# Performance work log

Measured on AMD Instinct MI355X. Metric: run time of the kernel, lower is better.

## Reference

```python
import jax, jax.numpy as jnp
import numpy as np

EPS_LN = 1e-5


def fwht(x):
    """Fast Walsh-Hadamard transform over the last axis (power-of-two length).
    Vectorized butterfly: log2(n) stages, each a reshape + add/sub."""
    orig_shape = x.shape
    n = orig_shape[-1]
    y = x.reshape(-1, n)
    h = 1
    while h < n:
        y = y.reshape(-1, n // (2 * h), 2, h)
        a = y[:, :, 0, :]
        b = y[:, :, 1, :]
        y = jnp.stack([a + b, a - b], axis=2).reshape(-1, n)
        h <<= 1
    return y.reshape(orig_shape)


def setup_inputs() -> dict:
    key = jax.random.key(0)
    kx, kw, kg = jax.random.split(key, 3)
    B, S, D_IN, D_OUT = 4, 4096, 2048, 2048
    x = jax.random.normal(kx, (B, S, D_IN), dtype=jnp.float32)
    # kaiming_uniform_(a=sqrt(5)) -> bound = 1/sqrt(in_features)
    bound = 1.0 / np.sqrt(D_IN)
    W = jax.random.uniform(kw, (D_OUT, D_IN), dtype=jnp.float32,
                           minval=-bound, maxval=bound)
    gamma = jnp.ones((D_IN,), dtype=jnp.float32)
    beta = jnp.zeros((D_IN,), dtype=jnp.float32)
    return {"x": x, "W": W, "gamma": gamma, "beta": beta}


def reference(x, W, gamma, beta):
    bits = 4
    max_val = (1 << (bits - 1)) - 1  # 7
    # LayerNorm over last dim
    mu = jnp.mean(x, axis=-1, keepdims=True)
    var = jnp.mean(jnp.square(x - mu), axis=-1, keepdims=True)
    x_ln = (x - mu) * jax.lax.rsqrt(var + EPS_LN) * gamma + beta
    # Activation fake-quant to `bits` bits (per-row absmax scale)
    x_scale = jnp.clip(jnp.max(jnp.abs(x_ln), axis=-1, keepdims=True), 1e-6, None)
    x_int = jnp.clip(jnp.round(x_ln * max_val / x_scale), -max_val, max_val)
    x_q = x_int * x_scale / max_val
    # Hadamard transform of quantized activations
    x_h = fwht(x_q)
    # Ternary weight quantization with global mean-abs scale
    w_scale = jnp.clip(jnp.mean(jnp.abs(W)), 1e-6, None)
    w_q = (jnp.where(W > 0.5 * w_scale, 1.0, 0.0)
           + jnp.where(W < -0.5 * w_scale, -1.0, 0.0)) * w_scale
    # Linear (no bias), then second Hadamard transform
    out = jnp.einsum('bsd,od->bso', x_h, w_q)
    return fwht(out)
```

## Files before the change

### kernel.cpp

```cpp
#include <hip/hip_runtime.h>

typedef unsigned short u16;
typedef __attribute__((ext_vector_type(8))) __bf16 bf16x8;
typedef __attribute__((ext_vector_type(4))) float floatx4;

#define DDIM 2048
#define MROWS 16384

__device__ __forceinline__ u16 f2bf(float f) {
    unsigned int u = __builtin_bit_cast(unsigned int, f);
    u = (u + 0x7fffu + ((u >> 16) & 1u)) >> 16;
    return (u16)u;
}

__device__ __forceinline__ float wave_sum(float v) {
#pragma unroll
    for (int o = 32; o > 0; o >>= 1) v += __shfl_down(v, o, 64);
    return v;
}
__device__ __forceinline__ float wave_max(float v) {
#pragma unroll
    for (int o = 32; o > 0; o >>= 1) v = fmaxf(v, __shfl_down(v, o, 64));
    return v;
}

__global__ __launch_bounds__(256) void absmean_part(const float4* __restrict__ W4,
                                                    float* __restrict__ partial) {
    float s = 0.f;
    for (int i = blockIdx.x * 256 + threadIdx.x; i < (DDIM * DDIM / 4); i += 1024 * 256) {
        float4 v = W4[i];
        s += fabsf(v.x) + fabsf(v.y) + fabsf(v.z) + fabsf(v.w);
    }
    s = wave_sum(s);
    __shared__ float red[4];
    if ((threadIdx.x & 63) == 0) red[threadIdx.x >> 6] = s;
    __syncthreads();
    if (threadIdx.x == 0) partial[blockIdx.x] = red[0] + red[1] + red[2] + red[3];
}

template <bool QUANT>
__global__ __launch_bounds__(256) void transpose_k(const float* __restrict__ in,
                                                   float* __restrict__ out,
                                                   const float* __restrict__ partial) {
    __shared__ float tile[64][65];
    const int t = threadIdx.x;
    float wsc = 0.f, half_t = 0.f;
    if (QUANT) {
        __shared__ float wred[4];
        float s = partial[t] + partial[t + 256] + partial[t + 512] + partial[t + 768];
        s = wave_sum(s);
        if ((t & 63) == 0) wred[t >> 6] = s;
        __syncthreads();
        float m = (wred[0] + wred[1] + wred[2] + wred[3]) * (1.0f / (float)(DDIM * DDIM));
        wsc = fmaxf(m, 1e-6f);
        half_t = 0.5f * wsc;
        __syncthreads();
    }
    const int tx = t & 63;
    const int ty = t >> 6;
    const int r0 = blockIdx.y * 64;
    const int c0 = blockIdx.x * 64;
#pragma unroll
    for (int i = 0; i < 16; ++i) {
        int r = ty + i * 4;
        float w = in[(size_t)(r0 + r) * DDIM + c0 + tx];
        if (QUANT) w = (w > half_t ? wsc : 0.f) + (w < -half_t ? -wsc : 0.f);
        tile[r][tx] = w;
    }
    __syncthreads();
#pragma unroll
    for (int i = 0; i < 16; ++i) {
        int r = ty + i * 4;
        out[(size_t)(c0 + r) * DDIM + r0 + tx] = tile[tx][r];
    }
}

template <bool BF16OUT>
__global__ __launch_bounds__(256) void fwht_rows(const float* __restrict__ in,
                                                 void* __restrict__ out) {
    __shared__ float s0[DDIM];
    __shared__ float s1[DDIM];
    const int row = blockIdx.x;
    const int t = threadIdx.x;
    const int lane = t & 63;
    const float4* rp = (const float4*)(in + (size_t)row * DDIM);
    float4 a = rp[t], b = rp[t + 256];
    float v[8] = {a.x, a.y, a.z, a.w, b.x, b.y, b.z, b.w};

#pragma unroll
    for (int h = 1; h <= 4; h <<= 1)
#pragma unroll
        for (int j = 0; j < 8; ++j)
            if (!(j & h)) { float x = v[j], y = v[j | h]; v[j] = x + y; v[j | h] = x - y; }

#pragma unroll
    for (int m = 1; m <= 32; m <<= 1)
#pragma unroll
        for (int j = 0; j < 8; ++j) {
            float p = __shfl_xor(v[j], m, 64);
            v[j] = (lane & m) ? (p - v[j]) : (p + v[j]);
        }

    ((float4*)s0)[2 * t] = make_float4(v[0], v[1], v[2], v[3]);
    ((float4*)s0)[2 * t + 1] = make_float4(v[4], v[5], v[6], v[7]);
    __syncthreads();
    {
        int p1 = t ^ 64;
        float4 pa = ((const float4*)s0)[2 * p1], pb = ((const float4*)s0)[2 * p1 + 1];
        float pv[8] = {pa.x, pa.y, pa.z, pa.w, pb.x, pb.y, pb.z, pb.w};
#pragma unroll
        for (int j = 0; j < 8; ++j) v[j] = (t & 64) ? (pv[j] - v[j]) : (pv[j] + v[j]);
    }
    ((float4*)s1)[2 * t] = make_float4(v[0], v[1], v[2], v[3]);
    ((float4*)s1)[2 * t + 1] = make_float4(v[4], v[5], v[6], v[7]);
    __syncthreads();
    {
        int p2 = t ^ 128;
        float4 pa = ((const float4*)s1)[2 * p2], pb = ((const float4*)s1)[2 * p2 + 1];
        float pv[8] = {pa.x, pa.y, pa.z, pa.w, pb.x, pb.y, pb.z, pb.w};
#pragma unroll
        for (int j = 0; j < 8; ++j) v[j] = (t & 128) ? (pv[j] - v[j]) : (pv[j] + v[j]);
    }

    if (BF16OUT) {
        u16* op = (u16*)out + (size_t)row * DDIM;
        uint2 o0, o1;
        o0.x = (unsigned)f2bf(v[0]) | ((unsigned)f2bf(v[1]) << 16);
        o0.y = (unsigned)f2bf(v[2]) | ((unsigned)f2bf(v[3]) << 16);
        o1.x = (unsigned)f2bf(v[4]) | ((unsigned)f2bf(v[5]) << 16);
        o1.y = (unsigned)f2bf(v[6]) | ((unsigned)f2bf(v[7]) << 16);
        ((uint2*)op)[t] = o0;
        ((uint2*)op)[t + 256] = o1;
    } else {
        float* op = (float*)out + (size_t)row * DDIM;
        ((float4*)op)[t] = make_float4(v[0], v[1], v[2], v[3]);
        ((float4*)op)[t + 256] = make_float4(v[4], v[5], v[6], v[7]);
    }
}

__global__ __launch_bounds__(256) void ln_quant(const float* __restrict__ X,
                                                const float* __restrict__ G,
                                                const float* __restrict__ Bt,
                                                u16* __restrict__ XQ) {
    const int row = blockIdx.x;
    const int t = threadIdx.x;
    const float4* rp = (const float4*)(X + (size_t)row * DDIM);
    float4 v0 = rp[t], v1 = rp[t + 256];
    float v[8] = {v0.x, v0.y, v0.z, v0.w, v1.x, v1.y, v1.z, v1.w};

    __shared__ float redA[4], redB[4], redC[4];
    const int wv = t >> 6, ln = t & 63;

    float s = 0.f, s2 = 0.f;
#pragma unroll
    for (int j = 0; j < 8; ++j) { s += v[j]; s2 += v[j] * v[j]; }
#pragma unroll
    for (int o = 32; o > 0; o >>= 1) {
        s += __shfl_down(s, o, 64);
        s2 += __shfl_down(s2, o, 64);
    }
    if (ln == 0) { redA[wv] = s; redB[wv] = s2; }
    __syncthreads();
    const float mu = (redA[0] + redA[1] + redA[2] + redA[3]) * (1.f / (float)DDIM);
    const float ex2 = (redB[0] + redB[1] + redB[2] + redB[3]) * (1.f / (float)DDIM);
    const float var = ex2 - mu * mu;
    const float rstd = rsqrtf(var + 1e-5f);

    const float4* gp = (const float4*)G;
    const float4* bp = (const float4*)Bt;
    float4 g0 = gp[t], g1 = gp[t + 256];
    float4 b0 = bp[t], b1 = bp[t + 256];
    float gg[8] = {g0.x, g0.y, g0.z, g0.w, g1.x, g1.y, g1.z, g1.w};
    float bb[8] = {b0.x, b0.y, b0.z, b0.w, b1.x, b1.y, b1.z, b1.w};

    float y[8];
    float am = 0.f;
#pragma unroll
    for (int j = 0; j < 8; ++j) {
        y[j] = (v[j] - mu) * rstd * gg[j] + bb[j];
        am = fmaxf(am, fabsf(y[j]));
    }
    float w = wave_max(am);
    if (ln == 0) redC[wv] = w;
    __syncthreads();
    const float scale = fmaxf(fmaxf(fmaxf(redC[0], redC[1]), fmaxf(redC[2], redC[3])), 1e-6f);

    const float r7 = 7.f / scale, s7 = scale / 7.f;
    unsigned int q[4];
#pragma unroll
    for (int j = 0; j < 8; j += 2) {
        float qa = fminf(fmaxf(rintf(y[j] * r7), -7.f), 7.f);
        float qb = fminf(fmaxf(rintf(y[j + 1] * r7), -7.f), 7.f);
        q[j >> 1] = (unsigned)f2bf(qa * s7) | ((unsigned)f2bf(qb * s7) << 16);
    }
    uint2 o0, o1;
    o0.x = q[0]; o0.y = q[1]; o1.x = q[2]; o1.y = q[3];
    uint2* orow = (uint2*)(XQ + (size_t)row * DDIM);
    orow[t] = o0;
    orow[t + 256] = o1;
}

#define GBK 64
#define GNT (DDIM / GBK)
#define TILEU (256 * GBK)

__device__ __forceinline__ void gl_lds16(const u16* g, u16* l) {
    __builtin_amdgcn_global_load_lds((const __attribute__((address_space(1))) void*)g,
                                     (__attribute__((address_space(3))) void*)l,
                                     16, 0, 0);
}

__device__ __forceinline__ void pbar() {
    __builtin_amdgcn_sched_barrier(0);
    asm volatile("" ::: "memory");
    __builtin_amdgcn_s_barrier();
    asm volatile("" ::: "memory");
    __builtin_amdgcn_sched_barrier(0);
}

__global__ __launch_bounds__(512, 2) void gemm256(const u16* __restrict__ A,
                                                  const u16* __restrict__ B,
                                                  float* __restrict__ C) {
    extern __shared__ __align__(16) u16 lds[];
    const int t = threadIdx.x;
    const int lane = t & 63;
    const int wid = t >> 6;
    const int wm = wid >> 2;
    const int wn = wid & 3;

    const int d = blockIdx.x;
    const int bm = (d & 7) | ((d >> 6) << 3);
    const int bn = (d >> 3) & 7;

    const int l15 = lane & 15;
    const int kq = lane >> 4;
    const int x7 = lane & 7;
    const int c0 = (kq ^ x7) << 3;
    const int c1 = ((kq | 4) ^ x7) << 3;
    const int arow = (wm << 7) + l15;
    const int brow = (wn << 6) + l15;

    const int srow = t >> 3;
    const int gch = ((t & 7) ^ (srow & 7)) << 3;
    const u16* Ag = A + (size_t)(bm * 256 + srow) * DDIM + gch;
    const u16* Bg = B + (size_t)(bn * 256 + srow) * DDIM + gch;

    floatx4 acc[8][4];
#pragma unroll
    for (int i = 0; i < 8; ++i)
#pragma unroll
        for (int j = 0; j < 4; ++j)
#pragma unroll
            for (int e = 0; e < 4; ++e) acc[i][j][e] = 0.f;

    bf16x8 a[4][2], b0v[2][2], b1v[2][2];

#define STAGE(gb, ldsoff, ko)                                                  \
    _Pragma("unroll") for (int q = 0; q < 4; ++q)                              \
        gl_lds16((gb) + (size_t)(q * 64) * DDIM + (ko),                        \
                 lds + (ldsoff) + q * 4096 + t * 8);

#define LDA(mh)                                                                \
    _Pragma("unroll") for (int fm = 0; fm < 4; ++fm) {                         \
        const u16* p = Ab + (arow + (mh) * 64 + fm * 16) * GBK;                \
        a[fm][0] = *(const bf16x8*)(p + c0);                                   \
        a[fm][1] = *(const bf16x8*)(p + c1);                                   \
    }

#define LDB(dst, nh)                                                           \
    _Pragma("unroll") for (int fn = 0; fn < 2; ++fn) {                         \
        const u16* p = Bb + (brow + (nh) * 32 + fn * 16) * GBK;                \
        dst[fn][0] = *(const bf16x8*)(p + c0);                                 \
        dst[fn][1] = *(const bf16x8*)(p + c1);                                 \
    }

#define MMA(mh, bsrc, nh)                                                      \
    __builtin_amdgcn_s_setprio(1);                                             \
    _Pragma("unroll") for (int fm = 0; fm < 4; ++fm)                           \
        _Pragma("unroll") for (int fn = 0; fn < 2; ++fn)                       \
            _Pragma("unroll") for (int ks = 0; ks < 2; ++ks)                   \
                acc[(mh) * 4 + fm][(nh) * 2 + fn] =                            \
                    __builtin_amdgcn_mfma_f32_16x16x32_bf16(                   \
                        a[fm][ks], bsrc[fn][ks],                               \
                        acc[(mh) * 4 + fm][(nh) * 2 + fn], 0, 0, 0);           \
    __builtin_amdgcn_s_setprio(0);

    STAGE(Ag, 0, 0);
    STAGE(Bg, TILEU, 0);
    STAGE(Ag, 2 * TILEU, GBK);
    STAGE(Bg, 3 * TILEU, GBK);
    __builtin_amdgcn_sched_barrier(0);
    asm volatile("s_waitcnt vmcnt(8)");
    pbar();

    for (int kt = 0; kt < GNT; ++kt) {
        const int boff = (kt & 1) * (2 * TILEU);
        const u16* Ab = lds + boff;
        const u16* Bb = lds + boff + TILEU;

        LDA(0);
        LDB(b0v, 0);
        pbar();
        MMA(0, b0v, 0);
        pbar();
        LDB(b1v, 1);
        pbar();
        MMA(0, b1v, 1);
        pbar();
        LDA(1);
        if (kt + 2 < GNT) { STAGE(Bg, boff + TILEU, (kt + 2) * GBK); }
        pbar();
        MMA(1, b0v, 0);
        pbar();
        if (kt + 2 < GNT) { STAGE(Ag, boff, (kt + 2) * GBK); }
        pbar();
        MMA(1, b1v, 1);
        __builtin_amdgcn_sched_barrier(0);
        if (kt < GNT - 2) {
            asm volatile("s_waitcnt vmcnt(8)");
        } else {
            asm volatile("s_waitcnt vmcnt(0)");
        }
        pbar();
    }

#undef STAGE
#undef LDA
#undef LDB
#undef MMA

    float* Cb = C + (size_t)(bm * 256 + (wm << 7) + (lane >> 4) * 4) * DDIM
                  + bn * 256 + (wn << 6) + l15;
#pragma unroll
    for (int fm = 0; fm < 8; ++fm)
#pragma unroll
        for (int fn = 0; fn < 4; ++fn)
#pragma unroll
            for (int r = 0; r < 4; ++r)
                Cb[(size_t)(fm * 16 + r) * DDIM + fn * 16] = acc[fm][fn][r];
}

extern "C" void kernel_launch(void* const* d_in, const int* in_sizes, int n_in,
                              void* d_out, int out_size, void* d_ws, size_t ws_size,
                              hipStream_t stream) {
    const float* X  = (const float*)d_in[0];
    const float* W  = (const float*)d_in[1];
    const float* G  = (const float*)d_in[2];
    const float* Bt = (const float*)d_in[3];
    float* out = (float*)d_out;

    char* ws = (char*)d_ws;
    u16*   xq   = (u16*)ws;
    float* bufA = (float*)(ws + (size_t)67108864);
    float* bufB = (float*)(ws + (size_t)67108864 + 16777216);
    float* partial = bufB;
    u16*   w3      = (u16*)bufB;

    absmean_part<<<1024, 256, 0, stream>>>((const float4*)W, partial);
    transpose_k<true><<<dim3(32, 32), 256, 0, stream>>>(W, bufA, partial);
    fwht_rows<false><<<2048, 256, 0, stream>>>(bufA, (void*)bufB);
    transpose_k<false><<<dim3(32, 32), 256, 0, stream>>>(bufB, bufA, nullptr);
    fwht_rows<true><<<2048, 256, 0, stream>>>(bufA, (void*)w3);
    ln_quant<<<MROWS, 256, 0, stream>>>(X, G, Bt, xq);
    hipFuncSetAttribute(reinterpret_cast<const void*>(gemm256),
                        hipFuncAttributeMaxDynamicSharedMemorySize, 131072);
    gemm256<<<dim3(512), 512, 131072, stream>>>(xq, w3, out);
}
```

Baseline: 398.2 us.

## Restructure GEMM main loop with 2x unroll, fused waits and interleaved prefetch

```diff
diff --git a/kernel.cpp b/kernel.cpp
--- a/kernel.cpp
+++ b/kernel.cpp
@@ -202,6 +202,7 @@
 
 #define GBK 64
 #define GNT (DDIM / GBK)
+#define NITER (GNT / 2)
 #define TILEU (256 * GBK)
 
 __device__ __forceinline__ void gl_lds16(const u16* g, u16* l) {
@@ -210,13 +211,29 @@
                                      16, 0, 0);
 }
 
-__device__ __forceinline__ void pbar() {
-    __builtin_amdgcn_sched_barrier(0);
-    asm volatile("" ::: "memory");
-    __builtin_amdgcn_s_barrier();
-    asm volatile("" ::: "memory");
-    __builtin_amdgcn_sched_barrier(0);
-}
+#define PBAR do {                                                              \
+    __builtin_amdgcn_sched_barrier(0);                                         \
+    asm volatile("" ::: "memory");                                             \
+    __builtin_amdgcn_s_barrier();                                              \
+    asm volatile("" ::: "memory");                                             \
+    __builtin_amdgcn_sched_barrier(0);                                         \
+} while (0)
+
+#define PWAIT8 do {                                                            \
+    __builtin_amdgcn_sched_barrier(0);                                         \
+    asm volatile("s_waitcnt vmcnt(8)" ::: "memory");                           \
+    __builtin_amdgcn_s_barrier();                                              \
+    asm volatile("" ::: "memory");                                             \
+    __builtin_amdgcn_sched_barrier(0);                                         \
+} while (0)
+
+#define PWAIT0 do {                                                            \
+    __builtin_amdgcn_sched_barrier(0);                                         \
+    asm volatile("s_waitcnt vmcnt(0)" ::: "memory");                           \
+    __builtin_amdgcn_s_barrier();                                              \
+    asm volatile("" ::: "memory");                                             \
+    __builtin_amdgcn_sched_barrier(0);                                         \
+} while (0)
 
 __global__ __launch_bounds__(512, 2) void gemm256(const u16* __restrict__ A,
                                                   const u16* __restrict__ B,
@@ -244,6 +261,14 @@
     const int gch = ((t & 7) ^ (srow & 7)) << 3;
     const u16* Ag = A + (size_t)(bm * 256 + srow) * DDIM + gch;
     const u16* Bg = B + (size_t)(bn * 256 + srow) * DDIM + gch;
+    u16* const AL0 = lds + t * 8;
+    u16* const BL0 = lds + TILEU + t * 8;
+    u16* const AL1 = lds + 2 * TILEU + t * 8;
+    u16* const BL1 = lds + 3 * TILEU + t * 8;
+    const u16* const Ab0 = lds;
+    const u16* const Bb0 = lds + TILEU;
+    const u16* const Ab1 = lds + 2 * TILEU;
+    const u16* const Bb1 = lds + 3 * TILEU;
 
     floatx4 acc[8][4];
 #pragma unroll
@@ -255,21 +280,19 @@
 
     bf16x8 a[4][2], b0v[2][2], b1v[2][2];
 
-#define STAGE(gb, ldsoff, ko)                                                  \
-    _Pragma("unroll") for (int q = 0; q < 4; ++q)                              \
-        gl_lds16((gb) + (size_t)(q * 64) * DDIM + (ko),                        \
-                 lds + (ldsoff) + q * 4096 + t * 8);
-
-#define LDA(mh)                                                                \
+#define STGA(dst, q, ko) gl_lds16(Ag + (size_t)((q) * 64) * DDIM + (ko), (dst) + (q) * 4096)
+#define STGB(dst, q, ko) gl_lds16(Bg + (size_t)((q) * 64) * DDIM + (ko), (dst) + (q) * 4096)
+
+#define LDA(Ab, mh)                                                            \
     _Pragma("unroll") for (int fm = 0; fm < 4; ++fm) {                         \
-        const u16* p = Ab + (arow + (mh) * 64 + fm * 16) * GBK;                \
+        const u16* p = (Ab) + (arow + (mh) * 64 + fm * 16) * GBK;              \
         a[fm][0] = *(const bf16x8*)(p + c0);                                   \
         a[fm][1] = *(const bf16x8*)(p + c1);                                   \
     }
 
-#define LDB(dst, nh)                                                           \
+#define LDB(dst, Bb, nh)                                                       \
     _Pragma("unroll") for (int fn = 0; fn < 2; ++fn) {                         \
-        const u16* p = Bb + (brow + (nh) * 32 + fn * 16) * GBK;                \
+        const u16* p = (Bb) + (brow + (nh) * 32 + fn * 16) * GBK;              \
         dst[fn][0] = *(const bf16x8*)(p + c0);                                 \
         dst[fn][1] = *(const bf16x8*)(p + c1);                                 \
     }
@@ -285,46 +308,56 @@
                         acc[(mh) * 4 + fm][(nh) * 2 + fn], 0, 0, 0);           \
     __builtin_amdgcn_s_setprio(0);
 
-    STAGE(Ag, 0, 0);
-    STAGE(Bg, TILEU, 0);
-    STAGE(Ag, 2 * TILEU, GBK);
-    STAGE(Bg, 3 * TILEU, GBK);
-    __builtin_amdgcn_sched_barrier(0);
-    asm volatile("s_waitcnt vmcnt(8)");
-    pbar();
-
-    for (int kt = 0; kt < GNT; ++kt) {
-        const int boff = (kt & 1) * (2 * TILEU);
-        const u16* Ab = lds + boff;
-        const u16* Bb = lds + boff + TILEU;
-
-        LDA(0);
-        LDB(b0v, 0);
-        pbar();
+#pragma unroll
+    for (int q = 0; q < 4; ++q) STGA(AL0, q, 0);
+#pragma unroll
+    for (int q = 0; q < 4; ++q) STGB(BL0, q, 0);
+#pragma unroll
+    for (int q = 0; q < 4; ++q) STGA(AL1, q, GBK);
+#pragma unroll
+    for (int q = 0; q < 4; ++q) STGB(BL1, q, GBK);
+    PWAIT8;
+
+    for (int it = 0; it < NITER; ++it) {
+        const int kp0 = (it * 2 + 2) * GBK;
+        const int kp1 = kp0 + GBK;
+        const bool pf = (it < NITER - 1);
+
+        LDA(Ab0, 0);
+        LDB(b0v, Bb0, 0);
+        PBAR;
         MMA(0, b0v, 0);
-        pbar();
-        LDB(b1v, 1);
-        pbar();
+        LDB(b1v, Bb0, 1);
+        if (pf) { STGA(AL0, 0, kp0); STGA(AL0, 2, kp0); }
+        PBAR;
         MMA(0, b1v, 1);
-        pbar();
-        LDA(1);
-        if (kt + 2 < GNT) { STAGE(Bg, boff + TILEU, (kt + 2) * GBK); }
-        pbar();
+        LDA(Ab0, 1);
+        if (pf) { STGB(BL0, 0, kp0); STGB(BL0, 1, kp0); }
+        PBAR;
         MMA(1, b0v, 0);
-        pbar();
-        if (kt + 2 < GNT) { STAGE(Ag, boff, (kt + 2) * GBK); }
-        pbar();
+        if (pf) { STGB(BL0, 2, kp0); STGB(BL0, 3, kp0); STGA(AL0, 1, kp0); STGA(AL0, 3, kp0); }
+        if (pf) { PWAIT8; } else { PWAIT0; }
         MMA(1, b1v, 1);
-        __builtin_amdgcn_sched_barrier(0);
-        if (kt < GNT - 2) {
-            asm volatile("s_waitcnt vmcnt(8)");
-        } else {
-            asm volatile("s_waitcnt vmcnt(0)");
-        }
-        pbar();
-    }
-
-#undef STAGE
+
+        LDA(Ab1, 0);
+        LDB(b0v, Bb1, 0);
+        PBAR;
+        MMA(0, b0v, 0);
+        LDB(b1v, Bb1, 1);
+        if (pf) { STGA(AL1, 0, kp1); STGA(AL1, 2, kp1); }
+        PBAR;
+        MMA(0, b1v, 1);
+        LDA(Ab1, 1);
+        if (pf) { STGB(BL1, 0, kp1); STGB(BL1, 1, kp1); }
+        PBAR;
+        MMA(1, b0v, 0);
+        if (pf) { STGB(BL1, 2, kp1); STGB(BL1, 3, kp1); STGA(AL1, 1, kp1); STGA(AL1, 3, kp1); }
+        if (pf) { PWAIT8; } else { PWAIT0; }
+        MMA(1, b1v, 1);
+    }
+
+#undef STGA
+#undef STGB
 #undef LDA
 #undef LDB
 #undef MMA
```

Result: faster. 377.0 us (-5.3%).
